# Kernel tuning notes

Hardware: AMD Instinct MI355X
Metric: run time of the kernel (lower is better)

## Reference

```python
import jax, jax.numpy as jnp
import numpy as np

BLK = 128            # weight_block_size for w8a16 blockwise dequant
H = 1024             # hidden_size
I = 512              # moe_intermediate_size
E = 64               # n_routed_experts
T = 512              # tokens (seq_len)
K = 6                # num_experts_per_tok
G = 8                # n_group
TG = 3               # topk_group
NSH = 2              # n_shared_experts
I2 = I * NSH         # shared expert intermediate size
ROUTED_SCALE = 2.5
NORM_TOPK = True


def dq(w_int8, scale, blk=BLK):
    """Blockwise w8a16 dequant: w [..., M, N] int8, scale [..., M/blk, N/blk] f32."""
    *lead, M, N = w_int8.shape
    w = w_int8.astype(scale.dtype).reshape(*lead, M // blk, blk, N // blk, blk)
    return (w * scale[..., :, None, :, None]).reshape(*lead, M, N)


def setup_inputs() -> dict:
    key = jax.random.key(0)
    ks = jax.random.split(key, 16)
    ri = lambda k, shp: jax.random.randint(k, shp, -8, 8, dtype=jnp.int8)
    rs = lambda k, shp: jax.random.uniform(k, shp, minval=0.01, maxval=0.03, dtype=jnp.float32)
    return {
        "x": jax.random.normal(ks[0], (T, H), jnp.float32),
        "gate_w": jax.random.normal(ks[1], (E, H), jnp.float32) * 0.02,  # router gate [E,H]
        "wg": ri(ks[2], (E, I, H)),  "sg": rs(ks[3], (E, I // BLK, H // BLK)),
        "wu": ri(ks[4], (E, I, H)),  "su": rs(ks[5], (E, I // BLK, H // BLK)),
        "wd": ri(ks[6], (E, I, H)),  "sd": rs(ks[7], (E, I // BLK, H // BLK)),  # down, transposed layout [I,H]
        "sh_wg": ri(ks[8], (I2, H)),  "sh_sg": rs(ks[9], (I2 // BLK, H // BLK)),
        "sh_wu": ri(ks[10], (I2, H)), "sh_su": rs(ks[11], (I2 // BLK, H // BLK)),
        "sh_wd": ri(ks[12], (I2, H)), "sh_sd": rs(ks[13], (I2 // BLK, H // BLK)),
    }


def _moe(x, gate_w, wg, sg, wu, su, wd, sd, sh_wg, sh_sg, sh_wu, sh_su, sh_wd, sh_sd):
    Tn = x.shape[0]
    # --- router: sigmoid scoring + group-limited top-k ---
    scores = jax.nn.sigmoid(x @ gate_w.T)                       # [T, E]
    gsz = E // G
    group_scores = scores.reshape(Tn, G, gsz).max(axis=-1)      # [T, G]
    _, gidx = jax.lax.top_k(group_scores, TG)                   # [T, TG]
    gmask = jax.nn.one_hot(gidx, G, dtype=scores.dtype).sum(1)  # [T, G]
    emask = jnp.repeat(gmask, gsz, axis=-1)                     # [T, E]
    masked = jnp.where(emask > 0, scores, -jnp.inf)
    w, idx = jax.lax.top_k(masked, K)                           # [T, K]
    if NORM_TOPK:
        w = w / (w.sum(-1, keepdims=True) + 1e-20)
    w = w * ROUTED_SCALE
    # per-token combine weights over experts
    comb = (jax.nn.one_hot(idx, E, dtype=x.dtype) * w[:, :, None]).sum(1)  # [T, E]

    # --- routed experts: dequantized silu-gated MLPs, masked dense combine ---
    Wg, Wu, Wd = dq(wg, sg), dq(wu, su), dq(wd, sd)             # [E, I, H]
    g = jnp.einsum('th,eih->eti', x, Wg)                        # [E, T, I]
    u = jnp.einsum('th,eih->eti', x, Wu)
    hmid = jax.nn.silu(g) * u
    y = jnp.einsum('eti,eih->eth', hmid, Wd)                    # [E, T, H]
    routed = jnp.einsum('eth,te->th', y, comb)                  # [T, H]

    # --- shared experts MLP ---
    Sg, Su, Sd = dq(sh_wg, sh_sg), dq(sh_wu, sh_su), dq(sh_wd, sh_sd)
    shared = (jax.nn.silu(x @ Sg.T) * (x @ Su.T)) @ Sd          # [T, H]
    return routed + shared


def reference(x, gate_w, wg, sg, wu, su, wd, sd, sh_wg, sh_sg, sh_wu, sh_su, sh_wd, sh_sd):
    return _moe(x, gate_w, wg, sg, wu, su, wd, sd,
                sh_wg, sh_sg, sh_wu, sh_su, sh_wd, sh_sd)
```

## Files before the change

### kernel.cpp

```cpp
#include <hip/hip_runtime.h>
#include <math.h>
#include <stdint.h>

#define T_   512
#define H_   1024
#define I_   512
#define E_   64
#define K_   6
#define G_   8
#define TG_  3
#define EB_  80

typedef _Float16 h8 __attribute__((ext_vector_type(8)));
typedef _Float16 h4v __attribute__((ext_vector_type(4)));
typedef float    f4 __attribute__((ext_vector_type(4)));

__global__ __launch_bounds__(64) void router_k(
    const float* __restrict__ x, const float* __restrict__ gw,
    int* __restrict__ cnt, int* __restrict__ tlist, float* __restrict__ wlist)
{
  const int t   = blockIdx.x;
  const int tid = threadIdx.x;
  __shared__ float sx[H_];
  __shared__ float sc[E_];

  for (int h4 = tid; h4 < H_/4; h4 += 64)
    ((float4*)sx)[h4] = ((const float4*)(x + (size_t)t*H_))[h4];
  __syncthreads();

  const float* wr = gw + (size_t)tid * H_;
  float acc = 0.f;
  for (int h = 0; h < H_; h += 4) {
    float4 xv = *(const float4*)(sx + h);
    float4 wv = *(const float4*)(wr + h);
    acc = fmaf(xv.x, wv.x, acc); acc = fmaf(xv.y, wv.y, acc);
    acc = fmaf(xv.z, wv.z, acc); acc = fmaf(xv.w, wv.w, acc);
  }
  sc[tid] = 1.f / (1.f + expf(-acc));
  __syncthreads();

  if (tid == 0) {
    float gs[G_];
    #pragma unroll
    for (int g = 0; g < G_; g++) {
      float m = sc[g*8];
      #pragma unroll
      for (int j = 1; j < 8; j++) m = fmaxf(m, sc[g*8+j]);
      gs[g] = m;
    }
    unsigned gp = 0;
    for (int r = 0; r < TG_; r++) {
      int best = 0; float bv = -1e30f;
      for (int g = 0; g < G_; g++)
        if (!((gp >> g) & 1) && gs[g] > bv) { bv = gs[g]; best = g; }
      gp |= 1u << best;
    }
    int   eidx[K_]; float ew[K_];
    unsigned long long em = 0ull;
    float wsum = 0.f;
    for (int r = 0; r < K_; r++) {
      int best = 0; float bv = -1e30f;
      for (int e = 0; e < E_; e++) {
        if (!((gp >> (e >> 3)) & 1)) continue;
        if ((em >> e) & 1ull) continue;
        if (sc[e] > bv) { bv = sc[e]; best = e; }
      }
      em |= 1ull << best; eidx[r] = best; ew[r] = bv; wsum += bv;
    }
    const float inv = 2.5f / (wsum + 1e-20f);
    for (int r = 0; r < K_; r++) {
      int e = eidx[r];
      int pos = atomicAdd(&cnt[e], 1);
      tlist[e*T_ + pos] = (t << 13) | (t*K_ + r);
      wlist[e*T_ + pos] = ew[r] * inv;
    }
  }
}

__global__ void pseudo_init_k(int* cnt, int* tlist, float* wlist) {
  int s = blockIdx.x*256 + threadIdx.x;
  if (s == 0) { cnt[64] = T_; cnt[65] = T_; }
  if (s < 1024) {
    int e = 64 + (s >> 9);
    int t = s & 511;
    tlist[e*T_ + t] = (t << 13) | (3072 + s);
    wlist[e*T_ + t] = 1.0f;
  }
}

__global__ __launch_bounds__(256) void xh_prep_k(
    const float* __restrict__ x, _Float16* __restrict__ xh)
{
  int i = blockIdx.x*256 + threadIdx.x;
  float4 v = ((const float4*)x)[i];
  h4v o = { (_Float16)v.x, (_Float16)v.y, (_Float16)v.z, (_Float16)v.w };
  *(h4v*)(xh + (size_t)i*4) = o;
}

__device__ __forceinline__ void eb_decode(int eb, const int* cnt,
                                          int& e, int& lo, int& hi) {
  if (eb < E_) { e = eb; lo = 0; hi = cnt[e]; }
  else { int q = (eb - E_) & 7; e = E_ + ((eb - E_) >> 3); lo = q*64; hi = lo + 64; }
}

__device__ __forceinline__ h8 cvt8(int4 a, int4 b, float s) {
  union { _Float16 f[8]; h8 v; } t;
  t.f[0]=(_Float16)((float)a.x*s); t.f[1]=(_Float16)((float)a.y*s);
  t.f[2]=(_Float16)((float)a.z*s); t.f[3]=(_Float16)((float)a.w*s);
  t.f[4]=(_Float16)((float)b.x*s); t.f[5]=(_Float16)((float)b.y*s);
  t.f[6]=(_Float16)((float)b.z*s); t.f[7]=(_Float16)((float)b.w*s);
  return t.v;
}

#define NKT_G 32

#define GU_STEP(KT, WN)                                                       \
  do {                                                                        \
    asm volatile("s_waitcnt vmcnt(" #WN ") lgkmcnt(0)" ::: "memory");         \
    __builtin_amdgcn_sched_barrier(0);                                        \
    __builtin_amdgcn_s_barrier();                                             \
    __builtin_amdgcn_sched_barrier(0);                                        \
    if ((KT) + 1 < NKT_G)                                                     \
      *(h8*)(wdst + (((KT)+1)&1)*5120) =                                      \
          cvt8(Wr[((KT)+1)%3][0], Wr[((KT)+1)%3][1], sv[((KT)+1)>>2]);        \
    if ((KT) + 3 < NKT_G) {                                                   \
      Wr[((KT)+3)%3][0] = *(const int4*)(wsrc + ((KT)+3)*32);                 \
      Wr[((KT)+3)%3][1] = *(const int4*)(wsrc + ((KT)+3)*32 + 4);             \
    }                                                                         \
    {                                                                         \
      const _Float16* tb = lds0 + ((KT)&1)*5120;                              \
      h8 bg0 = *(const h8*)(tb + ro0);                                        \
      h8 bg1 = *(const h8*)(tb + ro1);                                        \
      h8 bu0 = *(const h8*)(tb + 2560 + ro0);                                 \
      h8 bu1 = *(const h8*)(tb + 2560 + ro1);                                 \
      accg0 = __builtin_amdgcn_mfma_f32_16x16x32_f16(Ar[(KT)%4], bg0, accg0, 0,0,0); \
      accg1 = __builtin_amdgcn_mfma_f32_16x16x32_f16(Ar[(KT)%4], bg1, accg1, 0,0,0); \
      accu0 = __builtin_amdgcn_mfma_f32_16x16x32_f16(Ar[(KT)%4], bu0, accu0, 0,0,0); \
      accu1 = __builtin_amdgcn_mfma_f32_16x16x32_f16(Ar[(KT)%4], bu1, accu1, 0,0,0); \
    }                                                                         \
    if ((KT) + 3 < NKT_G)                                                     \
      Ar[((KT)+3)%4] = *(const h8*)(ax + ((KT)+3)*32);                        \
  } while (0)

__global__ __launch_bounds__(512, 6) void gateup_k(
    const _Float16* __restrict__ xh,
    const int* __restrict__ wg, const float* __restrict__ sg,
    const int* __restrict__ wu, const float* __restrict__ su,
    const int* __restrict__ shwg, const float* __restrict__ shsg,
    const int* __restrict__ shwu, const float* __restrict__ shsu,
    const int* __restrict__ cnt, const int* __restrict__ tlist,
    const float* __restrict__ wlist,
    _Float16* __restrict__ hmid)
{
  const int ic = blockIdx.x;
  const int eb = blockIdx.y;
  int e, lo, hi;
  eb_decode(eb, cnt, e, lo, hi);
  if (hi <= lo) return;

  const int tid  = threadIdx.x;
  const int lane = tid & 63;
  const int wv   = tid >> 6;
  const int mr   = lane & 15;
  const int quad = lane >> 4;
  const int wm   = wv & 3;
  const int wn   = wv >> 2;

  const int *wgb, *wub; const float *sgp, *sup; int sib;
  if (e < E_) {
    wgb = wg + (size_t)e*I_*H_;  wub = wu + (size_t)e*I_*H_;
    sgp = sg + e*32;  sup = su + e*32;  sib = ic >> 1;
  } else {
    int hf = e - E_;
    wgb = shwg + (size_t)hf*512*H_;  wub = shwu + (size_t)hf*512*H_;
    sgp = shsg;  sup = shsu;  sib = hf*4 + (ic >> 1);
  }

  const int smat = tid >> 8;
  const int sr   = (tid >> 2) & 63;
  const int sseg = tid & 3;
  const int* wsrc = (smat ? wub : wgb) + (size_t)(ic*64 + sr)*H_ + sseg*8;
  const float* ssc = (smat ? sup : sgp) + sib*8;
  float sv[8];
  #pragma unroll
  for (int b = 0; b < 8; b++) sv[b] = ssc[b];

  __shared__ _Float16 wlds[2*2*64*40];
  __shared__ int stok[64]; __shared__ int srw[64]; __shared__ float swt[64];
  _Float16* lds0 = wlds;
  _Float16* wdst = wlds + smat*2560 + sr*40 + sseg*8;
  const int ro0 = (wn*32 + mr)*40 + quad*8;
  const int ro1 = ro0 + 16*40;

  int4 Wr[3][2];
  h8   Ar[4];

  for (int base = lo; base < hi; base += 64) {
    __syncthreads();
    if (tid < 64) {
      int slot = base + tid;
      if (slot < hi) {
        int ent = tlist[e*T_ + slot];
        stok[tid] = ent >> 13; srw[tid] = ent & 8191; swt[tid] = wlist[e*T_ + slot];
      } else { stok[tid] = -1; srw[tid] = 0; swt[tid] = 0.f; }
    }
    __syncthreads();

    int tk = stok[wm*16 + mr]; if (tk < 0) tk = 0;
    const _Float16* ax = xh + (size_t)tk*H_ + quad*8;

    f4 accg0 = (f4){0.f,0.f,0.f,0.f}, accg1 = accg0, accu0 = accg0, accu1 = accg0;

    Wr[0][0] = *(const int4*)(wsrc);      Wr[0][1] = *(const int4*)(wsrc + 4);
    Ar[0]    = *(const h8*)(ax);
    Wr[1][0] = *(const int4*)(wsrc + 32); Wr[1][1] = *(const int4*)(wsrc + 36);
    Ar[1]    = *(const h8*)(ax + 32);
    Wr[2][0] = *(const int4*)(wsrc + 64); Wr[2][1] = *(const int4*)(wsrc + 68);
    Ar[2]    = *(const h8*)(ax + 64);
    asm volatile("s_waitcnt vmcnt(7)" ::: "memory");
    __builtin_amdgcn_sched_barrier(0);
    *(h8*)(wdst) = cvt8(Wr[0][0], Wr[0][1], sv[0]);

    GU_STEP(0,4);  GU_STEP(1,4);  GU_STEP(2,4);  GU_STEP(3,4);
    GU_STEP(4,4);  GU_STEP(5,4);  GU_STEP(6,4);  GU_STEP(7,4);
    GU_STEP(8,4);  GU_STEP(9,4);  GU_STEP(10,4); GU_STEP(11,4);
    GU_STEP(12,4); GU_STEP(13,4); GU_STEP(14,4); GU_STEP(15,4);
    GU_STEP(16,4); GU_STEP(17,4); GU_STEP(18,4); GU_STEP(19,4);
    GU_STEP(20,4); GU_STEP(21,4); GU_STEP(22,4); GU_STEP(23,4);
    GU_STEP(24,4); GU_STEP(25,4); GU_STEP(26,4); GU_STEP(27,4);
    GU_STEP(28,4); GU_STEP(29,4); GU_STEP(30,1); GU_STEP(31,0);

    const int icol = ic*64 + wn*32 + mr;
    #pragma unroll
    for (int r = 0; r < 4; r++) {
      int sl = wm*16 + quad*4 + r;
      if (stok[sl] >= 0) {
        float wt = swt[sl];
        float g0 = accg0[r];
        float m0 = g0 / (1.f + expf(-g0)) * accu0[r] * wt;
        float g1 = accg1[r];
        float m1 = g1 / (1.f + expf(-g1)) * accu1[r] * wt;
        _Float16* hp = hmid + (size_t)srw[sl]*I_ + icol;
        hp[0]  = (_Float16)m0;
        hp[16] = (_Float16)m1;
      }
    }
  }
}
#undef GU_STEP

#define NKT_D 16

#define DN_LDW(S, KT)                                                         \
  do {                                                                        \
    Wr[S][0] = *(const int2*)(dsrc + (size_t)((KT)*32 + 0)*H_);               \
    Wr[S][1] = *(const int2*)(dsrc + (size_t)((KT)*32 + 1)*H_);               \
    Wr[S][2] = *(const int2*)(dsrc + (size_t)((KT)*32 + 2)*H_);               \
    Wr[S][3] = *(const int2*)(dsrc + (size_t)((KT)*32 + 3)*H_);               \
  } while (0)

#define DN_WRITE(S, BUF, SC)                                                  \
  do {                                                                        \
    union { _Float16 f[4]; h4v v; } v0, v1;                                   \
    v0.f[0]=(_Float16)((float)Wr[S][0].x*(SC)); v0.f[1]=(_Float16)((float)Wr[S][1].x*(SC)); \
    v0.f[2]=(_Float16)((float)Wr[S][2].x*(SC)); v0.f[3]=(_Float16)((float)Wr[S][3].x*(SC)); \
    v1.f[0]=(_Float16)((float)Wr[S][0].y*(SC)); v1.f[1]=(_Float16)((float)Wr[S][1].y*(SC)); \
    v1.f[2]=(_Float16)((float)Wr[S][2].y*(SC)); v1.f[3]=(_Float16)((float)Wr[S][3].y*(SC)); \
    *(h4v*)(ddst0 + (BUF)*2560)      = v0.v;                                  \
    *(h4v*)(ddst0 + (BUF)*2560 + 40) = v1.v;                                  \
  } while (0)

#define DN_STEP(KT, WN)                                                       \
  do {                                                                        \
    asm volatile("s_waitcnt vmcnt(" #WN ") lgkmcnt(0)" ::: "memory");         \
    __builtin_amdgcn_sched_barrier(0);                                        \
    __builtin_amdgcn_s_barrier();                                             \
    __builtin_amdgcn_sched_barrier(0);                                        \
    if ((KT) + 1 < NKT_D) DN_WRITE(((KT)+1)%3, ((KT)+1)&1, scd[((KT)+1)>>2]); \
    if ((KT) + 3 < NKT_D) DN_LDW(((KT)+3)%3, (KT)+3);                         \
    {                                                                         \
      const _Float16* tb = lds0 + ((KT)&1)*2560;                              \
      h8 b0 = *(const h8*)(tb + ro0);                                         \
      h8 b1 = *(const h8*)(tb + ro1);                                         \
      h8 b2 = *(const h8*)(tb + ro2);                                         \
      h8 b3 = *(const h8*)(tb + ro3);                                         \
      tot0 = __builtin_amdgcn_mfma_f32_16x16x32_f16(Ar[(KT)%4], b0, tot0, 0,0,0); \
      tot1 = __builtin_amdgcn_mfma_f32_16x16x32_f16(Ar[(KT)%4], b1, tot1, 0,0,0); \
      tot2 = __builtin_amdgcn_mfma_f32_16x16x32_f16(Ar[(KT)%4], b2, tot2, 0,0,0); \
      tot3 = __builtin_amdgcn_mfma_f32_16x16x32_f16(Ar[(KT)%4], b3, tot3, 0,0,0); \
    }                                                                         \
    if ((KT) + 3 < NKT_D)                                                     \
      Ar[((KT)+3)%4] = *(const h8*)(ap + ((KT)+3)*32);                        \
  } while (0)

__global__ __launch_bounds__(256, 6) void down_k(
    const int* __restrict__ wd, const float* __restrict__ sd,
    const int* __restrict__ shwd, const float* __restrict__ shsd,
    const int* __restrict__ cnt, const int* __restrict__ tlist,
    const _Float16* __restrict__ hmid, float* __restrict__ scr)
{
  const int hc = blockIdx.x;
  const int eb = blockIdx.y;
  int e, lo, hi;
  eb_decode(eb, cnt, e, lo, hi);
  if (hi <= lo) return;

  const int tid  = threadIdx.x;
  const int lane = tid & 63;
  const int wv   = tid >> 6;
  const int mr   = lane & 15;
  const int quad = lane >> 4;

  const int* wb; const float* sdp; int sib0;
  if (e < E_) { wb = wd + (size_t)e*I_*H_;        sdp = sd + e*32;  sib0 = 0; }
  else { int hf = e - E_; wb = shwd + (size_t)hf*512*H_; sdp = shsd; sib0 = hf*4; }
  float scd[4];
  #pragma unroll
  for (int ib = 0; ib < 4; ib++) scd[ib] = sdp[(sib0+ib)*8 + (hc >> 1)];

  const int ig = tid >> 5;
  const int hp = tid & 31;
  const int* dsrc = wb + (size_t)(ig*4)*H_ + hc*64 + hp*2;

  __shared__ _Float16 wlds[2*64*40];
  __shared__ int stok[64]; __shared__ int srw[64];
  _Float16* lds0  = wlds;
  _Float16* ddst0 = wlds + (hp*2)*40 + ig*4;
  const int ro0 = (     mr)*40 + quad*8;
  const int ro1 = (16 + mr)*40 + quad*8;
  const int ro2 = (32 + mr)*40 + quad*8;
  const int ro3 = (48 + mr)*40 + quad*8;

  int2 Wr[3][4];
  h8   Ar[4];

  for (int base = lo; base < hi; base += 64) {
    __syncthreads();
    if (tid < 64) {
      int slot = base + tid;
      if (slot < hi) {
        int ent = tlist[e*T_ + slot];
        stok[tid] = ent >> 13; srw[tid] = ent & 8191;
      } else { stok[tid] = -1; srw[tid] = 0; }
    }
    __syncthreads();

    const _Float16* ap = hmid + (size_t)srw[wv*16 + mr]*I_ + quad*8;

    f4 tot0 = (f4){0.f,0.f,0.f,0.f}, tot1 = tot0, tot2 = tot0, tot3 = tot0;

    DN_LDW(0, 0); Ar[0] = *(const h8*)(ap);
    DN_LDW(1, 1); Ar[1] = *(const h8*)(ap + 32);
    DN_LDW(2, 2); Ar[2] = *(const h8*)(ap + 64);
    asm volatile("s_waitcnt vmcnt(10)" ::: "memory");
    __builtin_amdgcn_sched_barrier(0);
    DN_WRITE(0, 0, scd[0]);

    DN_STEP(0,6);  DN_STEP(1,6);  DN_STEP(2,6);  DN_STEP(3,6);
    DN_STEP(4,6);  DN_STEP(5,6);  DN_STEP(6,6);  DN_STEP(7,6);
    DN_STEP(8,6);  DN_STEP(9,6);  DN_STEP(10,6); DN_STEP(11,6);
    DN_STEP(12,6); DN_STEP(13,6); DN_STEP(14,1); DN_STEP(15,0);

    #pragma unroll
    for (int r = 0; r < 4; r++) {
      int sl = wv*16 + quad*4 + r;
      if (stok[sl] >= 0) {
        int t  = stok[sl];
        int sr = srw[sl];
        int rank = (sr < 3072) ? (sr - t*6) : (6 + ((sr - 3072) >> 9));
        float* dst = scr + (size_t)(t*8 + rank)*H_ + hc*64 + mr;
        dst[0]  = tot0[r];
        dst[16] = tot1[r];
        dst[32] = tot2[r];
        dst[48] = tot3[r];
      }
    }
  }
}
#undef DN_STEP
#undef DN_WRITE
#undef DN_LDW

__global__ __launch_bounds__(256) void combine_k(
    const float* __restrict__ scr, float* __restrict__ out)
{
  int i = blockIdx.x*256 + threadIdx.x;
  int t = i >> 8;
  int c = i & 255;
  const float4* base = (const float4*)(scr + (size_t)t*8*H_) + c;
  float4 s = base[0];
  #pragma unroll
  for (int r = 1; r < 8; r++) {
    float4 v = base[(size_t)r*(H_/4)];
    s.x += v.x; s.y += v.y; s.z += v.z; s.w += v.w;
  }
  ((float4*)out)[i] = s;
}

extern "C" void kernel_launch(void* const* d_in, const int* in_sizes, int n_in,
                              void* d_out, int out_size, void* d_ws, size_t ws_size,
                              hipStream_t stream) {
  (void)in_sizes; (void)n_in; (void)ws_size; (void)out_size;
  const float* x    = (const float*)d_in[0];
  const float* gw   = (const float*)d_in[1];
  const int*   wg   = (const int*  )d_in[2];
  const float* sg   = (const float*)d_in[3];
  const int*   wu   = (const int*  )d_in[4];
  const float* su   = (const float*)d_in[5];
  const int*   wd   = (const int*  )d_in[6];
  const float* sd   = (const float*)d_in[7];
  const int*   shwg = (const int*  )d_in[8];
  const float* shsg = (const float*)d_in[9];
  const int*   shwu = (const int*  )d_in[10];
  const float* shsu = (const float*)d_in[11];
  const int*   shwd = (const int*  )d_in[12];
  const float* shsd = (const float*)d_in[13];
  float* out = (float*)d_out;

  char* ws = (char*)d_ws;
  int*      cnt   = (int*     ) ws;
  int*      tlist = (int*     )(ws + 1024);
  float*    wlist = (float*   )(ws + 1024 + 66*T_*4);
  _Float16* hmid  = (_Float16*)(ws + 1024 + 2*66*T_*4);
  _Float16* xh    = (_Float16*)(ws + 1024 + 2*66*T_*4 + 4096*I_*2);
  float*    scr   = (float*   )(ws + 1024 + 2*66*T_*4 + 4096*I_*2 + T_*H_*2);

  hipMemsetAsync(cnt, 0, 1024, stream);
  xh_prep_k<<<T_*H_/1024, 256, 0, stream>>>(x, xh);
  router_k<<<T_, 64, 0, stream>>>(x, gw, cnt, tlist, wlist);
  pseudo_init_k<<<4, 256, 0, stream>>>(cnt, tlist, wlist);
  gateup_k<<<dim3(8, EB_), 512, 0, stream>>>(xh, wg, sg, wu, su,
                                             shwg, shsg, shwu, shsu,
                                             cnt, tlist, wlist, hmid);
  down_k<<<dim3(16, EB_), 256, 0, stream>>>(wd, sd, shwd, shsd,
                                            cnt, tlist, hmid, scr);
  combine_k<<<T_*H_/1024, 256, 0, stream>>>(scr, out);
}
```

Baseline: 557.3 us.

## Split K dimension in gate-up and down GEMMs, fuse prep kernels into router

```diff
diff --git a/kernel.cpp b/kernel.cpp
--- a/kernel.cpp
+++ b/kernel.cpp
@@ -17,7 +17,8 @@
 
 __global__ __launch_bounds__(64) void router_k(
     const float* __restrict__ x, const float* __restrict__ gw,
-    int* __restrict__ cnt, int* __restrict__ tlist, float* __restrict__ wlist)
+    int* __restrict__ cnt, int* __restrict__ tlist,
+    float* __restrict__ wrow, _Float16* __restrict__ xh)
 {
   const int t   = blockIdx.x;
   const int tid = threadIdx.x;
@@ -27,6 +28,20 @@
   for (int h4 = tid; h4 < H_/4; h4 += 64)
     ((float4*)sx)[h4] = ((const float4*)(x + (size_t)t*H_))[h4];
   __syncthreads();
+
+  for (int h4 = tid; h4 < H_/4; h4 += 64) {
+    float4 v = ((const float4*)sx)[h4];
+    h4v o = { (_Float16)v.x, (_Float16)v.y, (_Float16)v.z, (_Float16)v.w };
+    *(h4v*)(xh + (size_t)t*H_ + h4*4) = o;
+  }
+  if (t < 16) {
+    int s  = t*64 + tid;
+    int e  = 64 + (s >> 9);
+    int tt = s & 511;
+    tlist[e*T_ + tt] = (tt << 13) | (3072 + s);
+    wrow[3072 + s] = 1.0f;
+    if (s == 0) { cnt[64] = T_; cnt[65] = T_; }
+  }
 
   const float* wr = gw + (size_t)tid * H_;
   float acc = 0.f;
@@ -72,29 +87,9 @@
       int e = eidx[r];
       int pos = atomicAdd(&cnt[e], 1);
       tlist[e*T_ + pos] = (t << 13) | (t*K_ + r);
-      wlist[e*T_ + pos] = ew[r] * inv;
-    }
-  }
-}
-
-__global__ void pseudo_init_k(int* cnt, int* tlist, float* wlist) {
-  int s = blockIdx.x*256 + threadIdx.x;
-  if (s == 0) { cnt[64] = T_; cnt[65] = T_; }
-  if (s < 1024) {
-    int e = 64 + (s >> 9);
-    int t = s & 511;
-    tlist[e*T_ + t] = (t << 13) | (3072 + s);
-    wlist[e*T_ + t] = 1.0f;
-  }
-}
-
-__global__ __launch_bounds__(256) void xh_prep_k(
-    const float* __restrict__ x, _Float16* __restrict__ xh)
-{
-  int i = blockIdx.x*256 + threadIdx.x;
-  float4 v = ((const float4*)x)[i];
-  h4v o = { (_Float16)v.x, (_Float16)v.y, (_Float16)v.z, (_Float16)v.w };
-  *(h4v*)(xh + (size_t)i*4) = o;
+      wrow[t*K_ + r] = ew[r] * inv;
+    }
+  }
 }
 
 __device__ __forceinline__ void eb_decode(int eb, const int* cnt,
@@ -112,7 +107,7 @@
   return t.v;
 }
 
-#define NKT_G 32
+#define NKT_G 16
 
 #define GU_STEP(KT, WN)                                                       \
   do {                                                                        \
@@ -122,7 +117,7 @@
     __builtin_amdgcn_sched_barrier(0);                                        \
     if ((KT) + 1 < NKT_G)                                                     \
       *(h8*)(wdst + (((KT)+1)&1)*5120) =                                      \
-          cvt8(Wr[((KT)+1)%3][0], Wr[((KT)+1)%3][1], sv[((KT)+1)>>2]);        \
+          cvt8(Wr[((KT)+1)%3][0], Wr[((KT)+1)%3][1], sv[(((KT)+1)>>2)&3]);    \
     if ((KT) + 3 < NKT_G) {                                                   \
       Wr[((KT)+3)%3][0] = *(const int4*)(wsrc + ((KT)+3)*32);                 \
       Wr[((KT)+3)%3][1] = *(const int4*)(wsrc + ((KT)+3)*32 + 4);             \
@@ -142,17 +137,18 @@
       Ar[((KT)+3)%4] = *(const h8*)(ax + ((KT)+3)*32);                        \
   } while (0)
 
-__global__ __launch_bounds__(512, 6) void gateup_k(
+__global__ __launch_bounds__(512, 8) void gateup_k(
     const _Float16* __restrict__ xh,
     const int* __restrict__ wg, const float* __restrict__ sg,
     const int* __restrict__ wu, const float* __restrict__ su,
     const int* __restrict__ shwg, const float* __restrict__ shsg,
     const int* __restrict__ shwu, const float* __restrict__ shsu,
     const int* __restrict__ cnt, const int* __restrict__ tlist,
-    const float* __restrict__ wlist,
-    _Float16* __restrict__ hmid)
+    float* __restrict__ gpart)
 {
-  const int ic = blockIdx.x;
+  const int bx = blockIdx.x;
+  const int ic = bx & 7;
+  const int kc = bx >> 3;
   const int eb = blockIdx.y;
   int e, lo, hi;
   eb_decode(eb, cnt, e, lo, hi);
@@ -179,18 +175,21 @@
   const int smat = tid >> 8;
   const int sr   = (tid >> 2) & 63;
   const int sseg = tid & 3;
-  const int* wsrc = (smat ? wub : wgb) + (size_t)(ic*64 + sr)*H_ + sseg*8;
-  const float* ssc = (smat ? sup : sgp) + sib*8;
-  float sv[8];
+  const int* wsrc = (smat ? wub : wgb) + (size_t)(ic*64 + sr)*H_ + kc*512 + sseg*8;
+  const float* ssc = (smat ? sup : sgp) + sib*8 + kc*4;
+  float sv[4];
   #pragma unroll
-  for (int b = 0; b < 8; b++) sv[b] = ssc[b];
+  for (int b = 0; b < 4; b++) sv[b] = ssc[b];
 
   __shared__ _Float16 wlds[2*2*64*40];
-  __shared__ int stok[64]; __shared__ int srw[64]; __shared__ float swt[64];
+  __shared__ int stok[64]; __shared__ int srw[64];
   _Float16* lds0 = wlds;
   _Float16* wdst = wlds + smat*2560 + sr*40 + sseg*8;
   const int ro0 = (wn*32 + mr)*40 + quad*8;
   const int ro1 = ro0 + 16*40;
+
+  float* gp = gpart + (size_t)(kc*2 + 0)*4096*512;
+  float* up = gpart + (size_t)(kc*2 + 1)*4096*512;
 
   int4 Wr[3][2];
   h8   Ar[4];
@@ -201,13 +200,13 @@
       int slot = base + tid;
       if (slot < hi) {
         int ent = tlist[e*T_ + slot];
-        stok[tid] = ent >> 13; srw[tid] = ent & 8191; swt[tid] = wlist[e*T_ + slot];
-      } else { stok[tid] = -1; srw[tid] = 0; swt[tid] = 0.f; }
+        stok[tid] = ent >> 13; srw[tid] = ent & 8191;
+      } else { stok[tid] = -1; srw[tid] = 0; }
     }
     __syncthreads();
 
     int tk = stok[wm*16 + mr]; if (tk < 0) tk = 0;
-    const _Float16* ax = xh + (size_t)tk*H_ + quad*8;
+    const _Float16* ax = xh + (size_t)tk*H_ + kc*512 + quad*8;
 
     f4 accg0 = (f4){0.f,0.f,0.f,0.f}, accg1 = accg0, accu0 = accg0, accu1 = accg0;
 
@@ -224,32 +223,47 @@
     GU_STEP(0,4);  GU_STEP(1,4);  GU_STEP(2,4);  GU_STEP(3,4);
     GU_STEP(4,4);  GU_STEP(5,4);  GU_STEP(6,4);  GU_STEP(7,4);
     GU_STEP(8,4);  GU_STEP(9,4);  GU_STEP(10,4); GU_STEP(11,4);
-    GU_STEP(12,4); GU_STEP(13,4); GU_STEP(14,4); GU_STEP(15,4);
-    GU_STEP(16,4); GU_STEP(17,4); GU_STEP(18,4); GU_STEP(19,4);
-    GU_STEP(20,4); GU_STEP(21,4); GU_STEP(22,4); GU_STEP(23,4);
-    GU_STEP(24,4); GU_STEP(25,4); GU_STEP(26,4); GU_STEP(27,4);
-    GU_STEP(28,4); GU_STEP(29,4); GU_STEP(30,1); GU_STEP(31,0);
+    GU_STEP(12,4); GU_STEP(13,4); GU_STEP(14,1); GU_STEP(15,0);
 
     const int icol = ic*64 + wn*32 + mr;
     #pragma unroll
     for (int r = 0; r < 4; r++) {
       int sl = wm*16 + quad*4 + r;
       if (stok[sl] >= 0) {
-        float wt = swt[sl];
-        float g0 = accg0[r];
-        float m0 = g0 / (1.f + expf(-g0)) * accu0[r] * wt;
-        float g1 = accg1[r];
-        float m1 = g1 / (1.f + expf(-g1)) * accu1[r] * wt;
-        _Float16* hp = hmid + (size_t)srw[sl]*I_ + icol;
-        hp[0]  = (_Float16)m0;
-        hp[16] = (_Float16)m1;
+        size_t ro = (size_t)srw[sl]*512 + icol;
+        gp[ro]      = accg0[r];
+        gp[ro + 16] = accg1[r];
+        up[ro]      = accu0[r];
+        up[ro + 16] = accu1[r];
       }
     }
   }
 }
 #undef GU_STEP
 
-#define NKT_D 16
+__global__ __launch_bounds__(256) void gu_fin_k(
+    const float* __restrict__ gpart, const float* __restrict__ wrow,
+    _Float16* __restrict__ hmid)
+{
+  int i = blockIdx.x*256 + threadIdx.x;
+  int row = i >> 7;
+  const float4* g0 = (const float4*)(gpart)                        + i;
+  const float4* u0 = (const float4*)(gpart + (size_t)1*4096*512)   + i;
+  const float4* g1 = (const float4*)(gpart + (size_t)2*4096*512)   + i;
+  const float4* u1 = (const float4*)(gpart + (size_t)3*4096*512)   + i;
+  float4 ga = *g0, gb = *g1, ua = *u0, ub = *u1;
+  float w = wrow[row];
+  union { _Float16 f[4]; h4v v; } o;
+  #pragma unroll
+  for (int j = 0; j < 4; j++) {
+    float g = (&ga.x)[j] + (&gb.x)[j];
+    float u = (&ua.x)[j] + (&ub.x)[j];
+    o.f[j] = (_Float16)(g / (1.f + expf(-g)) * u * w);
+  }
+  *(h4v*)(hmid + (size_t)i*4) = o.v;
+}
+
+#define NKT_D 8
 
 #define DN_LDW(S, KT)                                                         \
   do {                                                                        \
@@ -276,7 +290,7 @@
     __builtin_amdgcn_sched_barrier(0);                                        \
     __builtin_amdgcn_s_barrier();                                             \
     __builtin_amdgcn_sched_barrier(0);                                        \
-    if ((KT) + 1 < NKT_D) DN_WRITE(((KT)+1)%3, ((KT)+1)&1, scd[((KT)+1)>>2]); \
+    if ((KT) + 1 < NKT_D) DN_WRITE(((KT)+1)%3, ((KT)+1)&1, scd[(((KT)+1)>>2)&1]); \
     if ((KT) + 3 < NKT_D) DN_LDW(((KT)+3)%3, (KT)+3);                         \
     {                                                                         \
       const _Float16* tb = lds0 + ((KT)&1)*2560;                              \
@@ -299,7 +313,9 @@
     const int* __restrict__ cnt, const int* __restrict__ tlist,
     const _Float16* __restrict__ hmid, float* __restrict__ scr)
 {
-  const int hc = blockIdx.x;
+  const int bx = blockIdx.x;
+  const int hc = bx & 15;
+  const int kc = bx >> 4;
   const int eb = blockIdx.y;
   int e, lo, hi;
   eb_decode(eb, cnt, e, lo, hi);
@@ -314,13 +330,13 @@
   const int* wb; const float* sdp; int sib0;
   if (e < E_) { wb = wd + (size_t)e*I_*H_;        sdp = sd + e*32;  sib0 = 0; }
   else { int hf = e - E_; wb = shwd + (size_t)hf*512*H_; sdp = shsd; sib0 = hf*4; }
-  float scd[4];
+  float scd[2];
   #pragma unroll
-  for (int ib = 0; ib < 4; ib++) scd[ib] = sdp[(sib0+ib)*8 + (hc >> 1)];
+  for (int ib = 0; ib < 2; ib++) scd[ib] = sdp[(sib0 + kc*2 + ib)*8 + (hc >> 1)];
 
   const int ig = tid >> 5;
   const int hp = tid & 31;
-  const int* dsrc = wb + (size_t)(ig*4)*H_ + hc*64 + hp*2;
+  const int* dsrc = wb + (size_t)(kc*256 + ig*4)*H_ + hc*64 + hp*2;
 
   __shared__ _Float16 wlds[2*64*40];
   __shared__ int stok[64]; __shared__ int srw[64];
@@ -331,6 +347,8 @@
   const int ro2 = (32 + mr)*40 + quad*8;
   const int ro3 = (48 + mr)*40 + quad*8;
 
+  float* scrk = scr + (size_t)kc*4096*H_;
+
   int2 Wr[3][4];
   h8   Ar[4];
 
@@ -345,7 +363,7 @@
     }
     __syncthreads();
 
-    const _Float16* ap = hmid + (size_t)srw[wv*16 + mr]*I_ + quad*8;
+    const _Float16* ap = hmid + (size_t)srw[wv*16 + mr]*I_ + kc*256 + quad*8;
 
     f4 tot0 = (f4){0.f,0.f,0.f,0.f}, tot1 = tot0, tot2 = tot0, tot3 = tot0;
 
@@ -356,10 +374,8 @@
     __builtin_amdgcn_sched_barrier(0);
     DN_WRITE(0, 0, scd[0]);
 
-    DN_STEP(0,6);  DN_STEP(1,6);  DN_STEP(2,6);  DN_STEP(3,6);
-    DN_STEP(4,6);  DN_STEP(5,6);  DN_STEP(6,6);  DN_STEP(7,6);
-    DN_STEP(8,6);  DN_STEP(9,6);  DN_STEP(10,6); DN_STEP(11,6);
-    DN_STEP(12,6); DN_STEP(13,6); DN_STEP(14,1); DN_STEP(15,0);
+    DN_STEP(0,6); DN_STEP(1,6); DN_STEP(2,6); DN_STEP(3,6);
+    DN_STEP(4,6); DN_STEP(5,6); DN_STEP(6,1); DN_STEP(7,0);
 
     #pragma unroll
     for (int r = 0; r < 4; r++) {
@@ -368,7 +384,7 @@
         int t  = stok[sl];
         int sr = srw[sl];
         int rank = (sr < 3072) ? (sr - t*6) : (6 + ((sr - 3072) >> 9));
-        float* dst = scr + (size_t)(t*8 + rank)*H_ + hc*64 + mr;
+        float* dst = scrk + (size_t)(t*8 + rank)*H_ + hc*64 + mr;
         dst[0]  = tot0[r];
         dst[16] = tot1[r];
         dst[32] = tot2[r];
@@ -381,18 +397,21 @@
 #undef DN_WRITE
 #undef DN_LDW
 
-__global__ __launch_bounds__(256) void combine_k(
+__global__ __launch_bounds__(256) void dn_fin_k(
     const float* __restrict__ scr, float* __restrict__ out)
 {
   int i = blockIdx.x*256 + threadIdx.x;
   int t = i >> 8;
   int c = i & 255;
-  const float4* base = (const float4*)(scr + (size_t)t*8*H_) + c;
-  float4 s = base[0];
+  const float4* b0 = (const float4*)(scr)                      + (size_t)t*8*(H_/4) + c;
+  const float4* b1 = (const float4*)(scr + (size_t)4096*H_)    + (size_t)t*8*(H_/4) + c;
+  float4 s = {0.f, 0.f, 0.f, 0.f};
   #pragma unroll
-  for (int r = 1; r < 8; r++) {
-    float4 v = base[(size_t)r*(H_/4)];
-    s.x += v.x; s.y += v.y; s.z += v.z; s.w += v.w;
+  for (int r = 0; r < 8; r++) {
+    float4 v0 = b0[(size_t)r*(H_/4)];
+    float4 v1 = b1[(size_t)r*(H_/4)];
+    s.x += v0.x + v1.x; s.y += v0.y + v1.y;
+    s.z += v0.z + v1.z; s.w += v0.w + v1.w;
   }
   ((float4*)out)[i] = s;
 }
@@ -420,19 +439,18 @@
   char* ws = (char*)d_ws;
   int*      cnt   = (int*     ) ws;
   int*      tlist = (int*     )(ws + 1024);
-  float*    wlist = (float*   )(ws + 1024 + 66*T_*4);
-  _Float16* hmid  = (_Float16*)(ws + 1024 + 2*66*T_*4);
-  _Float16* xh    = (_Float16*)(ws + 1024 + 2*66*T_*4 + 4096*I_*2);
-  float*    scr   = (float*   )(ws + 1024 + 2*66*T_*4 + 4096*I_*2 + T_*H_*2);
+  float*    wrow  = (float*   )(ws + 136192);
+  _Float16* hmid  = (_Float16*)(ws + 152576);
+  _Float16* xh    = (_Float16*)(ws + 4346880);
+  float*    big   = (float*   )(ws + 5395456);
 
   hipMemsetAsync(cnt, 0, 1024, stream);
-  xh_prep_k<<<T_*H_/1024, 256, 0, stream>>>(x, xh);
-  router_k<<<T_, 64, 0, stream>>>(x, gw, cnt, tlist, wlist);
-  pseudo_init_k<<<4, 256, 0, stream>>>(cnt, tlist, wlist);
-  gateup_k<<<dim3(8, EB_), 512, 0, stream>>>(xh, wg, sg, wu, su,
-                                             shwg, shsg, shwu, shsu,
-                                             cnt, tlist, wlist, hmid);
-  down_k<<<dim3(16, EB_), 256, 0, stream>>>(wd, sd, shwd, shsd,
-                                            cnt, tlist, hmid, scr);
-  combine_k<<<T_*H_/1024, 256, 0, stream>>>(scr, out);
-}
+  router_k<<<T_, 64, 0, stream>>>(x, gw, cnt, tlist, wrow, xh);
+  gateup_k<<<dim3(16, EB_), 512, 0, stream>>>(xh, wg, sg, wu, su,
+                                              shwg, shsg, shwu, shsu,
+                                              cnt, tlist, big);
+  gu_fin_k<<<2048, 256, 0, stream>>>(big, wrow, hmid);
+  down_k<<<dim3(32, EB_), 256, 0, stream>>>(wd, sd, shwd, shsd,
+                                            cnt, tlist, hmid, big);
+  dn_fin_k<<<512, 256, 0, stream>>>(big, out);
+}
```

Result: faster. 538.3 us (-3.4%).

## Repack int32 weights to int8 per call and fuse prep kernels into router

Applied to the files above, without the earlier changes.

```diff
diff --git a/kernel.cpp b/kernel.cpp
--- a/kernel.cpp
+++ b/kernel.cpp
@@ -15,9 +15,17 @@
 typedef _Float16 h4v __attribute__((ext_vector_type(4)));
 typedef float    f4 __attribute__((ext_vector_type(4)));
 
+#define CW_WU   33554432u
+#define CW_WD   67108864u
+#define CW_SHG 100663296u
+#define CW_SHU 101711872u
+#define CW_SHD 102760448u
+#define CW_END 103809024u
+
 __global__ __launch_bounds__(64) void router_k(
     const float* __restrict__ x, const float* __restrict__ gw,
-    int* __restrict__ cnt, int* __restrict__ tlist, float* __restrict__ wlist)
+    int* __restrict__ cnt, int* __restrict__ tlist,
+    float* __restrict__ wrow, _Float16* __restrict__ xh)
 {
   const int t   = blockIdx.x;
   const int tid = threadIdx.x;
@@ -27,6 +35,20 @@
   for (int h4 = tid; h4 < H_/4; h4 += 64)
     ((float4*)sx)[h4] = ((const float4*)(x + (size_t)t*H_))[h4];
   __syncthreads();
+
+  for (int h4 = tid; h4 < H_/4; h4 += 64) {
+    float4 v = ((const float4*)sx)[h4];
+    h4v o = { (_Float16)v.x, (_Float16)v.y, (_Float16)v.z, (_Float16)v.w };
+    *(h4v*)(xh + (size_t)t*H_ + h4*4) = o;
+  }
+  if (t < 16) {
+    int s  = t*64 + tid;
+    int e  = 64 + (s >> 9);
+    int tt = s & 511;
+    tlist[e*T_ + tt] = (tt << 13) | (3072 + s);
+    wrow[3072 + s] = 1.0f;
+    if (s == 0) { cnt[64] = T_; cnt[65] = T_; }
+  }
 
   const float* wr = gw + (size_t)tid * H_;
   float acc = 0.f;
@@ -72,29 +94,33 @@
       int e = eidx[r];
       int pos = atomicAdd(&cnt[e], 1);
       tlist[e*T_ + pos] = (t << 13) | (t*K_ + r);
-      wlist[e*T_ + pos] = ew[r] * inv;
-    }
-  }
-}
-
-__global__ void pseudo_init_k(int* cnt, int* tlist, float* wlist) {
-  int s = blockIdx.x*256 + threadIdx.x;
-  if (s == 0) { cnt[64] = T_; cnt[65] = T_; }
-  if (s < 1024) {
-    int e = 64 + (s >> 9);
-    int t = s & 511;
-    tlist[e*T_ + t] = (t << 13) | (3072 + s);
-    wlist[e*T_ + t] = 1.0f;
-  }
-}
-
-__global__ __launch_bounds__(256) void xh_prep_k(
-    const float* __restrict__ x, _Float16* __restrict__ xh)
+      wrow[t*K_ + r] = ew[r] * inv;
+    }
+  }
+}
+
+__global__ __launch_bounds__(256) void compact_k(
+    const int* __restrict__ wg, const int* __restrict__ wu,
+    const int* __restrict__ wd, const int* __restrict__ shwg,
+    const int* __restrict__ shwu, const int* __restrict__ shwd,
+    signed char* __restrict__ cw)
 {
-  int i = blockIdx.x*256 + threadIdx.x;
-  float4 v = ((const float4*)x)[i];
-  h4v o = { (_Float16)v.x, (_Float16)v.y, (_Float16)v.z, (_Float16)v.w };
-  *(h4v*)(xh + (size_t)i*4) = o;
+  long m = (long)blockIdx.x*256 + threadIdx.x;
+  const int* src; signed char* dst; long lm;
+  if      (m < 2097152) { src = wg;   dst = cw;          lm = m; }
+  else if (m < 4194304) { src = wu;   dst = cw + CW_WU;  lm = m - 2097152; }
+  else if (m < 6291456) { src = wd;   dst = cw + CW_WD;  lm = m - 4194304; }
+  else if (m < 6356992) { src = shwg; dst = cw + CW_SHG; lm = m - 6291456; }
+  else if (m < 6422528) { src = shwu; dst = cw + CW_SHU; lm = m - 6356992; }
+  else                  { src = shwd; dst = cw + CW_SHD; lm = m - 6422528; }
+  const int4* s = (const int4*)(src) + lm*4;
+  int4 a = s[0], b = s[1], c = s[2], d = s[3];
+  unsigned p0 = (a.x&255u) | ((a.y&255u)<<8) | ((a.z&255u)<<16) | ((a.w&255u)<<24);
+  unsigned p1 = (b.x&255u) | ((b.y&255u)<<8) | ((b.z&255u)<<16) | ((b.w&255u)<<24);
+  unsigned p2 = (c.x&255u) | ((c.y&255u)<<8) | ((c.z&255u)<<16) | ((c.w&255u)<<24);
+  unsigned p3 = (d.x&255u) | ((d.y&255u)<<8) | ((d.z&255u)<<16) | ((d.w&255u)<<24);
+  int4 o = { (int)p0, (int)p1, (int)p2, (int)p3 };
+  *(int4*)(dst + lm*16) = o;
 }
 
 __device__ __forceinline__ void eb_decode(int eb, const int* cnt,
@@ -103,12 +129,16 @@
   else { int q = (eb - E_) & 7; e = E_ + ((eb - E_) >> 3); lo = q*64; hi = lo + 64; }
 }
 
-__device__ __forceinline__ h8 cvt8(int4 a, int4 b, float s) {
+__device__ __forceinline__ h8 cvt8b(int2 w, float s) {
   union { _Float16 f[8]; h8 v; } t;
-  t.f[0]=(_Float16)((float)a.x*s); t.f[1]=(_Float16)((float)a.y*s);
-  t.f[2]=(_Float16)((float)a.z*s); t.f[3]=(_Float16)((float)a.w*s);
-  t.f[4]=(_Float16)((float)b.x*s); t.f[5]=(_Float16)((float)b.y*s);
-  t.f[6]=(_Float16)((float)b.z*s); t.f[7]=(_Float16)((float)b.w*s);
+  t.f[0]=(_Float16)((float)((w.x<<24)>>24)*s);
+  t.f[1]=(_Float16)((float)((w.x<<16)>>24)*s);
+  t.f[2]=(_Float16)((float)((w.x<< 8)>>24)*s);
+  t.f[3]=(_Float16)((float)( w.x     >>24)*s);
+  t.f[4]=(_Float16)((float)((w.y<<24)>>24)*s);
+  t.f[5]=(_Float16)((float)((w.y<<16)>>24)*s);
+  t.f[6]=(_Float16)((float)((w.y<< 8)>>24)*s);
+  t.f[7]=(_Float16)((float)( w.y     >>24)*s);
   return t.v;
 }
 
@@ -122,11 +152,9 @@
     __builtin_amdgcn_sched_barrier(0);                                        \
     if ((KT) + 1 < NKT_G)                                                     \
       *(h8*)(wdst + (((KT)+1)&1)*5120) =                                      \
-          cvt8(Wr[((KT)+1)%3][0], Wr[((KT)+1)%3][1], sv[((KT)+1)>>2]);        \
-    if ((KT) + 3 < NKT_G) {                                                   \
-      Wr[((KT)+3)%3][0] = *(const int4*)(wsrc + ((KT)+3)*32);                 \
-      Wr[((KT)+3)%3][1] = *(const int4*)(wsrc + ((KT)+3)*32 + 4);             \
-    }                                                                         \
+          cvt8b(Wr[((KT)+1)%3], sv[((KT)+1)>>2]);                             \
+    if ((KT) + 3 < NKT_G)                                                     \
+      Wr[((KT)+3)%3] = *(const int2*)(wsrc + ((KT)+3)*32);                    \
     {                                                                         \
       const _Float16* tb = lds0 + ((KT)&1)*5120;                              \
       h8 bg0 = *(const h8*)(tb + ro0);                                        \
@@ -142,14 +170,12 @@
       Ar[((KT)+3)%4] = *(const h8*)(ax + ((KT)+3)*32);                        \
   } while (0)
 
-__global__ __launch_bounds__(512, 6) void gateup_k(
-    const _Float16* __restrict__ xh,
-    const int* __restrict__ wg, const float* __restrict__ sg,
-    const int* __restrict__ wu, const float* __restrict__ su,
-    const int* __restrict__ shwg, const float* __restrict__ shsg,
-    const int* __restrict__ shwu, const float* __restrict__ shsu,
+__global__ __launch_bounds__(512, 8) void gateup_k(
+    const _Float16* __restrict__ xh, const signed char* __restrict__ cw,
+    const float* __restrict__ sg, const float* __restrict__ su,
+    const float* __restrict__ shsg, const float* __restrict__ shsu,
     const int* __restrict__ cnt, const int* __restrict__ tlist,
-    const float* __restrict__ wlist,
+    const float* __restrict__ wrow,
     _Float16* __restrict__ hmid)
 {
   const int ic = blockIdx.x;
@@ -166,20 +192,22 @@
   const int wm   = wv & 3;
   const int wn   = wv >> 2;
 
-  const int *wgb, *wub; const float *sgp, *sup; int sib;
+  const signed char *wgb, *wub; const float *sgp, *sup; int sib;
   if (e < E_) {
-    wgb = wg + (size_t)e*I_*H_;  wub = wu + (size_t)e*I_*H_;
+    wgb = cw + (size_t)e*I_*H_;
+    wub = cw + CW_WU + (size_t)e*I_*H_;
     sgp = sg + e*32;  sup = su + e*32;  sib = ic >> 1;
   } else {
     int hf = e - E_;
-    wgb = shwg + (size_t)hf*512*H_;  wub = shwu + (size_t)hf*512*H_;
+    wgb = cw + CW_SHG + (size_t)hf*512*H_;
+    wub = cw + CW_SHU + (size_t)hf*512*H_;
     sgp = shsg;  sup = shsu;  sib = hf*4 + (ic >> 1);
   }
 
   const int smat = tid >> 8;
   const int sr   = (tid >> 2) & 63;
   const int sseg = tid & 3;
-  const int* wsrc = (smat ? wub : wgb) + (size_t)(ic*64 + sr)*H_ + sseg*8;
+  const signed char* wsrc = (smat ? wub : wgb) + (size_t)(ic*64 + sr)*H_ + sseg*8;
   const float* ssc = (smat ? sup : sgp) + sib*8;
   float sv[8];
   #pragma unroll
@@ -192,7 +220,7 @@
   const int ro0 = (wn*32 + mr)*40 + quad*8;
   const int ro1 = ro0 + 16*40;
 
-  int4 Wr[3][2];
+  int2 Wr[3];
   h8   Ar[4];
 
   for (int base = lo; base < hi; base += 64) {
@@ -201,7 +229,8 @@
       int slot = base + tid;
       if (slot < hi) {
         int ent = tlist[e*T_ + slot];
-        stok[tid] = ent >> 13; srw[tid] = ent & 8191; swt[tid] = wlist[e*T_ + slot];
+        stok[tid] = ent >> 13; srw[tid] = ent & 8191;
+        swt[tid]  = wrow[ent & 8191];
       } else { stok[tid] = -1; srw[tid] = 0; swt[tid] = 0.f; }
     }
     __syncthreads();
@@ -211,24 +240,21 @@
 
     f4 accg0 = (f4){0.f,0.f,0.f,0.f}, accg1 = accg0, accu0 = accg0, accu1 = accg0;
 
-    Wr[0][0] = *(const int4*)(wsrc);      Wr[0][1] = *(const int4*)(wsrc + 4);
-    Ar[0]    = *(const h8*)(ax);
-    Wr[1][0] = *(const int4*)(wsrc + 32); Wr[1][1] = *(const int4*)(wsrc + 36);
-    Ar[1]    = *(const h8*)(ax + 32);
-    Wr[2][0] = *(const int4*)(wsrc + 64); Wr[2][1] = *(const int4*)(wsrc + 68);
-    Ar[2]    = *(const h8*)(ax + 64);
-    asm volatile("s_waitcnt vmcnt(7)" ::: "memory");
+    Wr[0] = *(const int2*)(wsrc);        Ar[0] = *(const h8*)(ax);
+    Wr[1] = *(const int2*)(wsrc + 32);   Ar[1] = *(const h8*)(ax + 32);
+    Wr[2] = *(const int2*)(wsrc + 64);   Ar[2] = *(const h8*)(ax + 64);
+    asm volatile("s_waitcnt vmcnt(5)" ::: "memory");
     __builtin_amdgcn_sched_barrier(0);
-    *(h8*)(wdst) = cvt8(Wr[0][0], Wr[0][1], sv[0]);
-
-    GU_STEP(0,4);  GU_STEP(1,4);  GU_STEP(2,4);  GU_STEP(3,4);
-    GU_STEP(4,4);  GU_STEP(5,4);  GU_STEP(6,4);  GU_STEP(7,4);
-    GU_STEP(8,4);  GU_STEP(9,4);  GU_STEP(10,4); GU_STEP(11,4);
-    GU_STEP(12,4); GU_STEP(13,4); GU_STEP(14,4); GU_STEP(15,4);
-    GU_STEP(16,4); GU_STEP(17,4); GU_STEP(18,4); GU_STEP(19,4);
-    GU_STEP(20,4); GU_STEP(21,4); GU_STEP(22,4); GU_STEP(23,4);
-    GU_STEP(24,4); GU_STEP(25,4); GU_STEP(26,4); GU_STEP(27,4);
-    GU_STEP(28,4); GU_STEP(29,4); GU_STEP(30,1); GU_STEP(31,0);
+    *(h8*)(wdst) = cvt8b(Wr[0], sv[0]);
+
+    GU_STEP(0,3);  GU_STEP(1,3);  GU_STEP(2,3);  GU_STEP(3,3);
+    GU_STEP(4,3);  GU_STEP(5,3);  GU_STEP(6,3);  GU_STEP(7,3);
+    GU_STEP(8,3);  GU_STEP(9,3);  GU_STEP(10,3); GU_STEP(11,3);
+    GU_STEP(12,3); GU_STEP(13,3); GU_STEP(14,3); GU_STEP(15,3);
+    GU_STEP(16,3); GU_STEP(17,3); GU_STEP(18,3); GU_STEP(19,3);
+    GU_STEP(20,3); GU_STEP(21,3); GU_STEP(22,3); GU_STEP(23,3);
+    GU_STEP(24,3); GU_STEP(25,3); GU_STEP(26,3); GU_STEP(27,3);
+    GU_STEP(28,3); GU_STEP(29,3); GU_STEP(30,1); GU_STEP(31,0);
 
     const int icol = ic*64 + wn*32 + mr;
     #pragma unroll
@@ -253,19 +279,23 @@
 
 #define DN_LDW(S, KT)                                                         \
   do {                                                                        \
-    Wr[S][0] = *(const int2*)(dsrc + (size_t)((KT)*32 + 0)*H_);               \
-    Wr[S][1] = *(const int2*)(dsrc + (size_t)((KT)*32 + 1)*H_);               \
-    Wr[S][2] = *(const int2*)(dsrc + (size_t)((KT)*32 + 2)*H_);               \
-    Wr[S][3] = *(const int2*)(dsrc + (size_t)((KT)*32 + 3)*H_);               \
+    Wr[S][0] = *(const unsigned short*)(dsrc + (size_t)((KT)*32 + 0)*H_);     \
+    Wr[S][1] = *(const unsigned short*)(dsrc + (size_t)((KT)*32 + 1)*H_);     \
+    Wr[S][2] = *(const unsigned short*)(dsrc + (size_t)((KT)*32 + 2)*H_);     \
+    Wr[S][3] = *(const unsigned short*)(dsrc + (size_t)((KT)*32 + 3)*H_);     \
   } while (0)
 
 #define DN_WRITE(S, BUF, SC)                                                  \
   do {                                                                        \
     union { _Float16 f[4]; h4v v; } v0, v1;                                   \
-    v0.f[0]=(_Float16)((float)Wr[S][0].x*(SC)); v0.f[1]=(_Float16)((float)Wr[S][1].x*(SC)); \
-    v0.f[2]=(_Float16)((float)Wr[S][2].x*(SC)); v0.f[3]=(_Float16)((float)Wr[S][3].x*(SC)); \
-    v1.f[0]=(_Float16)((float)Wr[S][0].y*(SC)); v1.f[1]=(_Float16)((float)Wr[S][1].y*(SC)); \
-    v1.f[2]=(_Float16)((float)Wr[S][2].y*(SC)); v1.f[3]=(_Float16)((float)Wr[S][3].y*(SC)); \
+    v0.f[0]=(_Float16)((float)(signed char)(Wr[S][0]     )*(SC));             \
+    v0.f[1]=(_Float16)((float)(signed char)(Wr[S][1]     )*(SC));             \
+    v0.f[2]=(_Float16)((float)(signed char)(Wr[S][2]     )*(SC));             \
+    v0.f[3]=(_Float16)((float)(signed char)(Wr[S][3]     )*(SC));             \
+    v1.f[0]=(_Float16)((float)(signed char)(Wr[S][0] >> 8)*(SC));             \
+    v1.f[1]=(_Float16)((float)(signed char)(Wr[S][1] >> 8)*(SC));             \
+    v1.f[2]=(_Float16)((float)(signed char)(Wr[S][2] >> 8)*(SC));             \
+    v1.f[3]=(_Float16)((float)(signed char)(Wr[S][3] >> 8)*(SC));             \
     *(h4v*)(ddst0 + (BUF)*2560)      = v0.v;                                  \
     *(h4v*)(ddst0 + (BUF)*2560 + 40) = v1.v;                                  \
   } while (0)
@@ -294,8 +324,8 @@
   } while (0)
 
 __global__ __launch_bounds__(256, 6) void down_k(
-    const int* __restrict__ wd, const float* __restrict__ sd,
-    const int* __restrict__ shwd, const float* __restrict__ shsd,
+    const signed char* __restrict__ cw,
+    const float* __restrict__ sd, const float* __restrict__ shsd,
     const int* __restrict__ cnt, const int* __restrict__ tlist,
     const _Float16* __restrict__ hmid, float* __restrict__ scr)
 {
@@ -311,16 +341,16 @@
   const int mr   = lane & 15;
   const int quad = lane >> 4;
 
-  const int* wb; const float* sdp; int sib0;
-  if (e < E_) { wb = wd + (size_t)e*I_*H_;        sdp = sd + e*32;  sib0 = 0; }
-  else { int hf = e - E_; wb = shwd + (size_t)hf*512*H_; sdp = shsd; sib0 = hf*4; }
+  const signed char* wb; const float* sdp; int sib0;
+  if (e < E_) { wb = cw + CW_WD + (size_t)e*I_*H_; sdp = sd + e*32;  sib0 = 0; }
+  else { int hf = e - E_; wb = cw + CW_SHD + (size_t)hf*512*H_; sdp = shsd; sib0 = hf*4; }
   float scd[4];
   #pragma unroll
   for (int ib = 0; ib < 4; ib++) scd[ib] = sdp[(sib0+ib)*8 + (hc >> 1)];
 
   const int ig = tid >> 5;
   const int hp = tid & 31;
-  const int* dsrc = wb + (size_t)(ig*4)*H_ + hc*64 + hp*2;
+  const signed char* dsrc = wb + (size_t)(ig*4)*H_ + hc*64 + hp*2;
 
   __shared__ _Float16 wlds[2*64*40];
   __shared__ int stok[64]; __shared__ int srw[64];
@@ -331,8 +361,8 @@
   const int ro2 = (32 + mr)*40 + quad*8;
   const int ro3 = (48 + mr)*40 + quad*8;
 
-  int2 Wr[3][4];
-  h8   Ar[4];
+  unsigned short Wr[3][4];
+  h8 Ar[4];
 
   for (int base = lo; base < hi; base += 64) {
     __syncthreads();
@@ -418,21 +448,20 @@
   float* out = (float*)d_out;
 
   char* ws = (char*)d_ws;
-  int*      cnt   = (int*     ) ws;
-  int*      tlist = (int*     )(ws + 1024);
-  float*    wlist = (float*   )(ws + 1024 + 66*T_*4);
-  _Float16* hmid  = (_Float16*)(ws + 1024 + 2*66*T_*4);
-  _Float16* xh    = (_Float16*)(ws + 1024 + 2*66*T_*4 + 4096*I_*2);
-  float*    scr   = (float*   )(ws + 1024 + 2*66*T_*4 + 4096*I_*2 + T_*H_*2);
+  int*         cnt   = (int*        ) ws;
+  int*         tlist = (int*        )(ws + 1024);
+  float*       wrow  = (float*      )(ws + 136192);
+  _Float16*    hmid  = (_Float16*   )(ws + 152576);
+  _Float16*    xh    = (_Float16*   )(ws + 4346880);
+  float*       scr   = (float*      )(ws + 5395456);
+  signed char* cw    = (signed char*)(ws + 22172672);
 
   hipMemsetAsync(cnt, 0, 1024, stream);
-  xh_prep_k<<<T_*H_/1024, 256, 0, stream>>>(x, xh);
-  router_k<<<T_, 64, 0, stream>>>(x, gw, cnt, tlist, wlist);
-  pseudo_init_k<<<4, 256, 0, stream>>>(cnt, tlist, wlist);
-  gateup_k<<<dim3(8, EB_), 512, 0, stream>>>(xh, wg, sg, wu, su,
-                                             shwg, shsg, shwu, shsu,
-                                             cnt, tlist, wlist, hmid);
-  down_k<<<dim3(16, EB_), 256, 0, stream>>>(wd, sd, shwd, shsd,
+  compact_k<<<25344, 256, 0, stream>>>(wg, wu, wd, shwg, shwu, shwd, cw);
+  router_k<<<T_, 64, 0, stream>>>(x, gw, cnt, tlist, wrow, xh);
+  gateup_k<<<dim3(8, EB_), 512, 0, stream>>>(xh, cw, sg, su, shsg, shsu,
+                                             cnt, tlist, wrow, hmid);
+  down_k<<<dim3(16, EB_), 256, 0, stream>>>(cw, sd, shsd,
                                             cnt, tlist, hmid, scr);
-  combine_k<<<T_*H_/1024, 256, 0, stream>>>(scr, out);
-}
+  combine_k<<<512, 256, 0, stream>>>(scr, out);
+}
```

Result: slower. 596.8 us (+7.1%).
